# Performance work log

Measured on AMD Instinct MI355X. Metric: run time of the kernel, lower is better.

## Reference

```python
import jax, jax.numpy as jnp
import numpy as np

V = 32000      # vocab_size
CTX = 1024     # context_length
D = 768        # n_embd
H = 12         # n_heads
HD = D // H    # head_dim
L = 6          # n_layers
DFF = 4 * D
B, S = 2, 1024
EPS = 1e-5


def _layernorm(x, w, b):
    mu = jnp.mean(x, axis=-1, keepdims=True)
    var = jnp.mean(jnp.square(x - mu), axis=-1, keepdims=True)
    return (x - mu) * jax.lax.rsqrt(var + EPS) * w + b


def setup_inputs() -> dict:
    key = jax.random.key(0)
    ks = iter(jax.random.split(key, 32))
    s = 0.02
    idx = jax.random.randint(next(ks), (B, S), 0, V)
    p = {
        "idx": idx,
        "tok_emb": jax.random.normal(next(ks), (V, D), jnp.float32) * s,
        "pos_emb": jax.random.normal(next(ks), (CTX, D), jnp.float32) * s,
        "ln1_w": jnp.ones((L, D)), "ln1_b": jnp.zeros((L, D)),
        "Wq": jax.random.normal(next(ks), (L, D, D), jnp.float32) * s,
        "bq": jnp.zeros((L, D)),
        "Wk": jax.random.normal(next(ks), (L, D, D), jnp.float32) * s,
        "bk": jnp.zeros((L, D)),
        "Wv": jax.random.normal(next(ks), (L, D, D), jnp.float32) * s,
        "bv": jnp.zeros((L, D)),
        "Wo": jax.random.normal(next(ks), (L, D, D), jnp.float32) * s,
        "bo": jnp.zeros((L, D)),
        "ln2_w": jnp.ones((L, D)), "ln2_b": jnp.zeros((L, D)),
        "W1": jax.random.normal(next(ks), (L, D, DFF), jnp.float32) * s,
        "b1": jnp.zeros((L, DFF)),
        "W2": jax.random.normal(next(ks), (L, DFF, D), jnp.float32) * s,
        "b2": jnp.zeros((L, D)),
        "lnf_w": jnp.ones((D,)), "lnf_b": jnp.zeros((D,)),
        "lm_head_w": jax.random.normal(next(ks), (D, V), jnp.float32) * s,
    }
    return p


def _forward(idx, tok_emb, pos_emb, ln1_w, ln1_b, Wq, bq, Wk, bk, Wv, bv,
             Wo, bo, ln2_w, ln2_b, W1, b1, W2, b2, lnf_w, lnf_b, lm_head_w):
    b, s = idx.shape
    x = tok_emb[idx] + pos_emb[:s]  # [B,S,D]
    mask = jnp.tril(jnp.ones((s, s), dtype=bool))  # causal
    scale = 1.0 / np.sqrt(HD)
    for l in range(L):
        # --- attention ---
        h = _layernorm(x, ln1_w[l], ln1_b[l])
        q = (h @ Wq[l] + bq[l]).reshape(b, s, H, HD).transpose(0, 2, 1, 3)
        k = (h @ Wk[l] + bk[l]).reshape(b, s, H, HD).transpose(0, 2, 1, 3)
        v = (h @ Wv[l] + bv[l]).reshape(b, s, H, HD).transpose(0, 2, 1, 3)
        att = jnp.einsum('bhqd,bhkd->bhqk', q, k) * scale
        att = jnp.where(mask, att, -jnp.inf)
        att = jax.nn.softmax(att, axis=-1)
        y = jnp.einsum('bhqk,bhkd->bhqd', att, v)
        y = y.transpose(0, 2, 1, 3).reshape(b, s, D)
        x = x + y @ Wo[l] + bo[l]
        # --- MLP ---
        h2 = _layernorm(x, ln2_w[l], ln2_b[l])
        x = x + jax.nn.relu(h2 @ W1[l] + b1[l]) @ W2[l] + b2[l]
    logits = _layernorm(x, lnf_w, lnf_b) @ lm_head_w  # [B,S,V]
    return logits


def reference(idx, tok_emb, pos_emb, ln1_w, ln1_b, Wq, bq, Wk, bk, Wv, bv,
              Wo, bo, ln2_w, ln2_b, W1, b1, W2, b2, lnf_w, lnf_b, lm_head_w):
    return _forward(idx, tok_emb, pos_emb, ln1_w, ln1_b, Wq, bq, Wk, bk, Wv,
                    bv, Wo, bo, ln2_w, ln2_b, W1, b1, W2, b2, lnf_w, lnf_b,
                    lm_head_w)
```

## Files before the change

### kernel.cpp

```cpp
#include <hip/hip_runtime.h>
#include <hip/hip_bf16.h>
#include <math.h>

#define D 768
#define NH 12
#define HD 64
#define NL 6
#define DFF 3072
#define BB 2
#define SS 1024
#define NROWS (BB*SS)
#define VOCAB 32000
#define QKVN (3*D)
#define LN_EPS 1e-5f

typedef __attribute__((ext_vector_type(8))) short bf16x8;
typedef __attribute__((ext_vector_type(4))) float f32x4;

typedef __attribute__((address_space(1))) const unsigned char* gas_ptr;
typedef __attribute__((address_space(3))) unsigned char* las_ptr;

__device__ __forceinline__ void load_lds16(const void* g, void* l) {
    __builtin_amdgcn_global_load_lds((gas_ptr)g, (las_ptr)l, 16, 0, 0);
}

__device__ __forceinline__ void storeOut(float* p, float v) { *p = v; }
__device__ __forceinline__ void storeOut(__hip_bfloat16* p, float v) { *p = __float2bfloat16(v); }
__device__ __forceinline__ ushort f2bs(float f) {
    __hip_bfloat16 h = __float2bfloat16(f);
    return *(ushort*)&h;
}

#define WAIT_VMCNT(n) asm volatile("s_waitcnt vmcnt(" #n ")" ::: "memory")

__global__ void embed_kernel(const int* __restrict__ idx, const float* __restrict__ tok,
                             const float* __restrict__ pos, float* __restrict__ x) {
    int row = blockIdx.x;
    int s = row % SS;
    int t = idx[row];
    for (int c = threadIdx.x; c < D; c += blockDim.x)
        x[row*D + c] = tok[(size_t)t*D + c] + pos[s*D + c];
}

template<typename OT>
__global__ __launch_bounds__(256) void layernorm_kernel(const float* __restrict__ x,
                                                        const float* __restrict__ w,
                                                        const float* __restrict__ b,
                                                        OT* __restrict__ out) {
    int row = blockIdx.x;
    __shared__ float l1[4], l2[4];
    int base = row * D;
    float vals[3];
    float s1 = 0.f, s2 = 0.f;
#pragma unroll
    for (int i = 0; i < 3; i++) {
        float v = x[base + threadIdx.x + i*256];
        vals[i] = v; s1 += v; s2 += v*v;
    }
#pragma unroll
    for (int o = 32; o > 0; o >>= 1) {
        s1 += __shfl_down(s1, o, 64);
        s2 += __shfl_down(s2, o, 64);
    }
    if ((threadIdx.x & 63) == 0) { l1[threadIdx.x >> 6] = s1; l2[threadIdx.x >> 6] = s2; }
    __syncthreads();
    float sum   = l1[0] + l1[1] + l1[2] + l1[3];
    float sumsq = l2[0] + l2[1] + l2[2] + l2[3];
    float mu  = sum * (1.f / D);
    float var = sumsq * (1.f / D) - mu * mu;
    float inv = rsqrtf(var + LN_EPS);
#pragma unroll
    for (int i = 0; i < 3; i++) {
        int c = threadIdx.x + i*256;
        storeOut(&out[base + c], (vals[i] - mu) * inv * w[c] + b[c]);
    }
}

__global__ __launch_bounds__(256) void transpose_cvt(const float* __restrict__ src,
                                                     __hip_bfloat16* __restrict__ dst,
                                                     int K, int N,
                                                     size_t srcLayerStride, size_t dstLayerStride,
                                                     int dstRowOff) {
    int l = blockIdx.z;
    src += (size_t)l * srcLayerStride;
    dst += (size_t)l * dstLayerStride + (size_t)dstRowOff * K;
    __shared__ float t[32][33];
    int k0 = blockIdx.x*32, n0 = blockIdx.y*32;
    int tx = threadIdx.x & 31, ty = threadIdx.x >> 5;
    for (int i = ty; i < 32; i += 8) t[i][tx] = src[(size_t)(k0+i)*N + n0+tx];
    __syncthreads();
    for (int i = ty; i < 32; i += 8) dst[(size_t)(n0+i)*K + k0+tx] = __float2bfloat16(t[tx][i]);
}

__global__ __launch_bounds__(256) void qkvo_trans(const float* __restrict__ Wq,
                                                  const float* __restrict__ Wk,
                                                  const float* __restrict__ Wv,
                                                  const float* __restrict__ Wo,
                                                  __hip_bfloat16* __restrict__ qkvT,
                                                  __hip_bfloat16* __restrict__ WoT) {
    int z = blockIdx.z, l = z >> 2, m = z & 3;
    const float* src = (m==0 ? Wq : m==1 ? Wk : m==2 ? Wv : Wo) + (size_t)l*D*D;
    __hip_bfloat16* dst = (m < 3) ? qkvT + (size_t)l*QKVN*D + (size_t)m*D*D
                                  : WoT  + (size_t)l*D*D;
    __shared__ float t[32][33];
    int k0 = blockIdx.x*32, n0 = blockIdx.y*32;
    int tx = threadIdx.x & 31, ty = threadIdx.x >> 5;
    for (int i = ty; i < 32; i += 8) t[i][tx] = src[(size_t)(k0+i)*D + n0+tx];
    __syncthreads();
    for (int i = ty; i < 32; i += 8) dst[(size_t)(n0+i)*D + k0+tx] = __float2bfloat16(t[tx][i]);
}

__global__ void pack_qkv_bias(const float* __restrict__ bq, const float* __restrict__ bk,
                              const float* __restrict__ bv, float* __restrict__ dst) {
    int l = blockIdx.y;
    int i = blockIdx.x*256 + threadIdx.x;
    dst[l*QKVN + i]         = bq[l*D + i];
    dst[l*QKVN + D + i]     = bk[l*D + i];
    dst[l*QKVN + 2*D + i]   = bv[l*D + i];
}

#define GSTAGE(buf, k0) do {                                                     \
    _Pragma("unroll")                                                            \
    for (int i_ = 0; i_ < BM/64; i_++) {                                         \
        int rt_ = wid*(BM/4) + i_*16;                                            \
        load_lds16(A + (size_t)(bm + rt_ + lrow)*K + (k0) + lcol,                \
                   &As[buf][rt_][0]);                                            \
    }                                                                            \
    _Pragma("unroll")                                                            \
    for (int i_ = 0; i_ < BN/64; i_++) {                                         \
        int rt_ = wid*(BN/4) + i_*16;                                            \
        load_lds16(BT + (size_t)(bn + rt_ + lrow)*K + (k0) + lcol,               \
                   &Bs[buf][rt_][0]);                                            \
    } } while (0)

template<int BM, int BN, int CMAJ, typename OT, int RELU, int RESID, int HASB, int VSTORE>
__global__ __launch_bounds__(256) void gemm_mfma(const ushort* __restrict__ A,
                                                 const ushort* __restrict__ BT,
                                                 const float* __restrict__ bias,
                                                 const float* __restrict__ X,
                                                 OT* __restrict__ C,
                                                 ushort* __restrict__ vt,
                                                 int N, int K, int gx, int gy) {
    constexpr int WTM = BM/2, WTN = BN/2;
    constexpr int FRM = BM/32, FRN = BN/32;
    constexpr int LPS = BM/64 + BN/64;
    __shared__ ushort As[3][BM][32];
    __shared__ ushort Bs[3][BN][32];

    int id = blockIdx.x;
    int swz = (id & 7) * (gridDim.x >> 3) + (id >> 3);
    int bx, by;
    if (CMAJ) { bx = swz / gy; by = swz - bx * gy; }
    else      { by = swz / gx; bx = swz - by * gx; }
    int bm = by * BM, bn = bx * BN;

    int tid = threadIdx.x;
    int lane = tid & 63, wid = tid >> 6;
    int wr = wid >> 1, wc = wid & 1;
    int lrow = lane >> 2;
    int lcol = (((lane & 3) ^ (lrow & 3)) * 8);
    int fr = lane & 15, fc = lane >> 4;

    f32x4 acc[FRM][FRN];
#pragma unroll
    for (int i = 0; i < FRM; i++)
#pragma unroll
        for (int j = 0; j < FRN; j++)
#pragma unroll
            for (int r = 0; r < 4; r++) acc[i][j][r] = 0.f;

    const int NT = K / 32;
    GSTAGE(0, 0);
    GSTAGE(1, 32);

    int cur = 0;
    for (int t = 0; t < NT; t++) {
        if (t + 1 < NT) {
            if constexpr (LPS == 2) WAIT_VMCNT(2);
            else if constexpr (LPS == 3) WAIT_VMCNT(3);
            else WAIT_VMCNT(4);
        } else {
            WAIT_VMCNT(0);
        }
        __builtin_amdgcn_s_barrier();
        asm volatile("" ::: "memory");
        if (t + 2 < NT) {
            int nb = cur >= 1 ? cur - 1 : cur + 2;
            GSTAGE(nb, (t+2)*32);
        }
        bf16x8 af[FRM], bf[FRN];
#pragma unroll
        for (int mi = 0; mi < FRM; mi++)
            af[mi] = *(const bf16x8*)&As[cur][wr*WTM + mi*16 + fr][(fc ^ (fr & 3))*8];
#pragma unroll
        for (int ni = 0; ni < FRN; ni++)
            bf[ni] = *(const bf16x8*)&Bs[cur][wc*WTN + ni*16 + fr][(fc ^ (fr & 3))*8];
        __builtin_amdgcn_s_setprio(1);
#pragma unroll
        for (int mi = 0; mi < FRM; mi++)
#pragma unroll
            for (int ni = 0; ni < FRN; ni++)
                acc[mi][ni] = __builtin_amdgcn_mfma_f32_16x16x32_bf16(af[mi], bf[ni], acc[mi][ni], 0, 0, 0);
        __builtin_amdgcn_s_setprio(0);
        cur = cur < 2 ? cur + 1 : 0;
    }

    if (VSTORE && bn >= 2*D) {
        int hh = (bn - 2*D) / HD;
        int b  = bm >> 10;
        size_t vbase = ((size_t)(b*NH + hh)) * HD;
        int srow0 = (bm & (SS-1)) + wr*WTM + fc*4;
#pragma unroll
        for (int mi = 0; mi < FRM; mi++) {
#pragma unroll
            for (int ni = 0; ni < FRN; ni++) {
                int col = bn + wc*WTN + ni*16 + fr;
                int d   = wc*WTN + ni*16 + fr;
                float bv_ = bias[col];
                ushort4 u;
                u.x = f2bs(acc[mi][ni][0] + bv_);
                u.y = f2bs(acc[mi][ni][1] + bv_);
                u.z = f2bs(acc[mi][ni][2] + bv_);
                u.w = f2bs(acc[mi][ni][3] + bv_);
                *(ushort4*)&vt[(vbase + d)*SS + srow0 + mi*16] = u;
            }
        }
    } else {
#pragma unroll
        for (int mi = 0; mi < FRM; mi++) {
#pragma unroll
            for (int r = 0; r < 4; r++) {
                int row = bm + wr*WTM + mi*16 + fc*4 + r;
#pragma unroll
                for (int ni = 0; ni < FRN; ni++) {
                    int col = bn + wc*WTN + ni*16 + fr;
                    float v = acc[mi][ni][r];
                    if (HASB) v += bias[col];
                    if (RESID) v += X[(size_t)row * N + col];
                    if (RELU) v = fmaxf(v, 0.f);
                    storeOut(&C[(size_t)row * N + col], v);
                }
            }
        }
    }
}

#define KVSTAGE(buf, kv0) do {                                                   \
    _Pragma("unroll")                                                            \
    for (int j_ = 0; j_ < 2; j_++) {                                             \
        int r_ = w*16 + j_*8 + srow8;                                            \
        load_lds16(qkv + (size_t)(b*SS + (kv0) + r_)*QKVN + D + h*HD + schunk*8, \
                   &Ks[buf][w*16 + j_*8][0]);                                    \
        load_lds16(vt + ((size_t)(b*NH + h)*HD + r_)*SS + (kv0) + schunk*8,      \
                   &Vs[buf][w*16 + j_*8][0]);                                    \
    } } while (0)

__global__ __launch_bounds__(256) void attn_mfma(const ushort* __restrict__ qkv,
                                                 const ushort* __restrict__ vt,
                                                 __hip_bfloat16* __restrict__ y) {
    const int bx = blockIdx.x;
    const int qt = 15 - (bx & 15);
    const int h  = (bx >> 4) % NH;
    const int b  = bx / (16*NH);
    const int tid  = threadIdx.x;
    const int lane = tid & 63, w = tid >> 6;
    const int fr = lane & 15, fc = lane >> 4;

    __shared__ ushort Qs[64][64];
    __shared__ ushort Ks[2][64][64];
    __shared__ ushort Vs[2][64][64];
    __shared__ ushort Ps[4][16][72];

    const int q0 = qt * 64;
    const int srow8  = lane >> 3;
    const int schunk = (lane & 7) ^ srow8;

#pragma unroll
    for (int j = 0; j < 2; j++) {
        int r = w*16 + j*8 + srow8;
        load_lds16(qkv + (size_t)(b*SS + q0 + r)*QKVN + h*HD + schunk*8, &Qs[w*16 + j*8][0]);
    }
    KVSTAGE(0, 0);
    asm volatile("s_waitcnt vmcnt(0)" ::: "memory");
    __syncthreads();
    bf16x8 qf[2];
#pragma unroll
    for (int s = 0; s < 2; s++)
        qf[s] = *(const bf16x8*)&Qs[w*16 + fr][((s*4 + fc) ^ (fr & 7))*8];

    f32x4 oacc[4];
#pragma unroll
    for (int ni = 0; ni < 4; ni++)
#pragma unroll
        for (int r = 0; r < 4; r++) oacc[ni][r] = 0.f;
    float m[4] = {-INFINITY, -INFINITY, -INFINITY, -INFINITY};
    float l[4] = {0.f, 0.f, 0.f, 0.f};

    int cur = 0;
    for (int kt = 0; kt <= qt; kt++) {
        if (kt < qt) KVSTAGE(cur^1, (kt+1)*64);
        f32x4 sacc[4];
#pragma unroll
        for (int ni = 0; ni < 4; ni++)
#pragma unroll
            for (int r = 0; r < 4; r++) sacc[ni][r] = 0.f;
#pragma unroll
        for (int ni = 0; ni < 4; ni++)
#pragma unroll
            for (int s = 0; s < 2; s++) {
                bf16x8 kf = *(const bf16x8*)&Ks[cur][ni*16 + fr][((s*4 + fc) ^ (fr & 7))*8];
                sacc[ni] = __builtin_amdgcn_mfma_f32_16x16x32_bf16(qf[s], kf, sacc[ni], 0, 0, 0);
            }
        if (kt == qt) {
#pragma unroll
            for (int ni = 0; ni < 4; ni++)
#pragma unroll
                for (int r = 0; r < 4; r++) {
                    float v = sacc[ni][r] * 0.125f;
                    sacc[ni][r] = (ni*16 + fr > w*16 + fc*4 + r) ? -INFINITY : v;
                }
        } else {
#pragma unroll
            for (int ni = 0; ni < 4; ni++)
#pragma unroll
                for (int r = 0; r < 4; r++) sacc[ni][r] *= 0.125f;
        }
        float p[4][4];
#pragma unroll
        for (int r = 0; r < 4; r++) {
            float mx = fmaxf(fmaxf(sacc[0][r], sacc[1][r]), fmaxf(sacc[2][r], sacc[3][r]));
#pragma unroll
            for (int o = 1; o < 16; o <<= 1) mx = fmaxf(mx, __shfl_xor(mx, o, 64));
            float mn = fmaxf(m[r], mx);
            float fac = __expf(m[r] - mn);
            float rs = 0.f;
#pragma unroll
            for (int ni = 0; ni < 4; ni++) {
                float pv = __expf(sacc[ni][r] - mn);
                p[ni][r] = pv;
                rs += pv;
            }
#pragma unroll
            for (int o = 1; o < 16; o <<= 1) rs += __shfl_xor(rs, o, 64);
            l[r] = l[r] * fac + rs;
            m[r] = mn;
#pragma unroll
            for (int ni = 0; ni < 4; ni++) oacc[ni][r] *= fac;
        }
#pragma unroll
        for (int ni = 0; ni < 4; ni++)
#pragma unroll
            for (int r = 0; r < 4; r++)
                Ps[w][fc*4 + r][ni*16 + fr] = f2bs(p[ni][r]);
        bf16x8 pa[2];
#pragma unroll
        for (int s = 0; s < 2; s++) pa[s] = *(const bf16x8*)&Ps[w][fr][s*32 + fc*8];
#pragma unroll
        for (int ni = 0; ni < 4; ni++)
#pragma unroll
            for (int s = 0; s < 2; s++) {
                bf16x8 vf = *(const bf16x8*)&Vs[cur][ni*16 + fr][((s*4 + fc) ^ (fr & 7))*8];
                oacc[ni] = __builtin_amdgcn_mfma_f32_16x16x32_bf16(pa[s], vf, oacc[ni], 0, 0, 0);
            }
        asm volatile("s_waitcnt vmcnt(0)" ::: "memory");
        __syncthreads();
        cur ^= 1;
    }
#pragma unroll
    for (int r = 0; r < 4; r++) {
        float rinv = 1.f / l[r];
        int row = b*SS + q0 + w*16 + fc*4 + r;
#pragma unroll
        for (int ni = 0; ni < 4; ni++)
            y[(size_t)row*D + h*HD + ni*16 + fr] = __float2bfloat16(oacc[ni][r] * rinv);
    }
}

extern "C" void kernel_launch(void* const* d_in, const int* in_sizes, int n_in,
                              void* d_out, int out_size, void* d_ws, size_t ws_size,
                              hipStream_t stream) {
    const int*   idx  = (const int*)d_in[0];
    const float* tok  = (const float*)d_in[1];
    const float* pos  = (const float*)d_in[2];
    const float* ln1w = (const float*)d_in[3];
    const float* ln1b = (const float*)d_in[4];
    const float* Wq   = (const float*)d_in[5];
    const float* bq   = (const float*)d_in[6];
    const float* Wk   = (const float*)d_in[7];
    const float* bk   = (const float*)d_in[8];
    const float* Wv   = (const float*)d_in[9];
    const float* bv   = (const float*)d_in[10];
    const float* Wo   = (const float*)d_in[11];
    const float* bo   = (const float*)d_in[12];
    const float* ln2w = (const float*)d_in[13];
    const float* ln2b = (const float*)d_in[14];
    const float* W1   = (const float*)d_in[15];
    const float* b1   = (const float*)d_in[16];
    const float* W2   = (const float*)d_in[17];
    const float* b2   = (const float*)d_in[18];
    const float* lnfw = (const float*)d_in[19];
    const float* lnfb = (const float*)d_in[20];
    const float* lmw  = (const float*)d_in[21];
    float* out = (float*)d_out;

    char* p = (char*)d_ws;
    __hip_bfloat16* qkvT = (__hip_bfloat16*)p; p += (size_t)NL*QKVN*D*2;
    __hip_bfloat16* WoT  = (__hip_bfloat16*)p; p += (size_t)NL*D*D*2;
    __hip_bfloat16* W1T  = (__hip_bfloat16*)p; p += (size_t)NL*DFF*D*2;
    __hip_bfloat16* W2T  = (__hip_bfloat16*)p; p += (size_t)NL*D*DFF*2;
    __hip_bfloat16* lmT  = (__hip_bfloat16*)p; p += (size_t)VOCAB*D*2;
    float*          bqkv = (float*)p;          p += (size_t)NL*QKVN*4;
    float*          x    = (float*)p;          p += (size_t)NROWS*D*4;
    __hip_bfloat16* h    = (__hip_bfloat16*)p; p += (size_t)NROWS*D*2;
    __hip_bfloat16* qkv  = (__hip_bfloat16*)p; p += (size_t)NROWS*QKVN*2;
    __hip_bfloat16* vt   = (__hip_bfloat16*)p; p += (size_t)BB*NH*HD*SS*2;
    __hip_bfloat16* yb   = (__hip_bfloat16*)p; p += (size_t)NROWS*D*2;
    __hip_bfloat16* a1   = (__hip_bfloat16*)p; p += (size_t)NROWS*DFF*2;

    qkvo_trans<<<dim3(D/32, D/32, NL*4), 256, 0, stream>>>(Wq, Wk, Wv, Wo, qkvT, WoT);
    transpose_cvt<<<dim3(D/32, DFF/32, NL), 256, 0, stream>>>(W1, W1T, D, DFF, (size_t)D*DFF, (size_t)DFF*D, 0);
    transpose_cvt<<<dim3(DFF/32, D/32, NL), 256, 0, stream>>>(W2, W2T, DFF, D, (size_t)DFF*D, (size_t)D*DFF, 0);
    transpose_cvt<<<dim3(D/32, VOCAB/32, 1), 256, 0, stream>>>(lmw, lmT, D, VOCAB, 0, 0, 0);
    pack_qkv_bias<<<dim3(3, NL), 256, 0, stream>>>(bq, bk, bv, bqkv);

    embed_kernel<<<NROWS, 256, 0, stream>>>(idx, tok, pos, x);

    for (int l = 0; l < NL; l++) {
        layernorm_kernel<<<NROWS, 256, 0, stream>>>(x, ln1w + l*D, ln1b + l*D, h);
        gemm_mfma<128,64,0,__hip_bfloat16,0,0,1,1><<<576, 256, 0, stream>>>(
            (const ushort*)h, (const ushort*)(qkvT + (size_t)l*QKVN*D),
            bqkv + (size_t)l*QKVN, nullptr, qkv, (ushort*)vt, QKVN, D, QKVN/64, NROWS/128);
        attn_mfma<<<BB*NH*(SS/64), 256, 0, stream>>>((const ushort*)qkv, (const ushort*)vt, yb);
        gemm_mfma<64,64,0,float,0,1,1,0><<<384, 256, 0, stream>>>(
            (const ushort*)yb, (const ushort*)(WoT + (size_t)l*D*D),
            bo + (size_t)l*D, x, x, nullptr, D, D, D/64, NROWS/64);
        layernorm_kernel<<<NROWS, 256, 0, stream>>>(x, ln2w + l*D, ln2b + l*D, h);
        gemm_mfma<128,128,0,__hip_bfloat16,1,0,1,0><<<384, 256, 0, stream>>>(
            (const ushort*)h, (const ushort*)(W1T + (size_t)l*DFF*D),
            b1 + (size_t)l*DFF, nullptr, a1, nullptr, DFF, D, DFF/128, NROWS/128);
        gemm_mfma<64,64,0,float,0,1,1,0><<<384, 256, 0, stream>>>(
            (const ushort*)a1, (const ushort*)(W2T + (size_t)l*D*DFF),
            b2 + (size_t)l*D, x, x, nullptr, D, DFF, D/64, NROWS/64);
    }
    layernorm_kernel<<<NROWS, 256, 0, stream>>>(x, lnfw, lnfb, h);
    gemm_mfma<128,128,1,float,0,0,0,0><<<4000, 256, 0, stream>>>(
        (const ushort*)h, (const ushort*)lmT, nullptr, nullptr, out, nullptr, VOCAB, D,
        VOCAB/128, NROWS/128);
}
```

Baseline: 1.251 ms.

## Add 256x256 LM-head GEMM kernel and simplify generic GEMM to double buffering

Adds a dedicated LM-head GEMM that uses 256x256 tiles with 512 threads, a K-step of 64, XOR-swizzled LDS and two-stage prefetch, so each block reuses more data and fewer blocks are launched for the largest matmul. It also changes the generic gemm_mfma from a three-buffer pipeline with partial vmcnt waits to a plain double buffer that waits for all loads and syncs on every iteration. That second change may add stalls to every per-layer GEMM, while the large LM-head tile costs more registers and LDS per block and lowers occupancy.

```diff
diff --git a/kernel.cpp b/kernel.cpp
--- a/kernel.cpp
+++ b/kernel.cpp
@@ -143,9 +143,8 @@
                                                  int N, int K, int gx, int gy) {
     constexpr int WTM = BM/2, WTN = BN/2;
     constexpr int FRM = BM/32, FRN = BN/32;
-    constexpr int LPS = BM/64 + BN/64;
-    __shared__ ushort As[3][BM][32];
-    __shared__ ushort Bs[3][BN][32];
+    __shared__ ushort As[2][BM][32];
+    __shared__ ushort Bs[2][BN][32];
 
     int id = blockIdx.x;
     int swz = (id & 7) * (gridDim.x >> 3) + (id >> 3);
@@ -169,25 +168,13 @@
 #pragma unroll
             for (int r = 0; r < 4; r++) acc[i][j][r] = 0.f;
 
-    const int NT = K / 32;
     GSTAGE(0, 0);
-    GSTAGE(1, 32);
+    asm volatile("s_waitcnt vmcnt(0)" ::: "memory");
+    __syncthreads();
 
     int cur = 0;
-    for (int t = 0; t < NT; t++) {
-        if (t + 1 < NT) {
-            if constexpr (LPS == 2) WAIT_VMCNT(2);
-            else if constexpr (LPS == 3) WAIT_VMCNT(3);
-            else WAIT_VMCNT(4);
-        } else {
-            WAIT_VMCNT(0);
-        }
-        __builtin_amdgcn_s_barrier();
-        asm volatile("" ::: "memory");
-        if (t + 2 < NT) {
-            int nb = cur >= 1 ? cur - 1 : cur + 2;
-            GSTAGE(nb, (t+2)*32);
-        }
+    for (int t = 0; t < K/32; t++) {
+        if (t*32 + 32 < K) GSTAGE(cur^1, t*32 + 32);
         bf16x8 af[FRM], bf[FRN];
 #pragma unroll
         for (int mi = 0; mi < FRM; mi++)
@@ -202,7 +189,9 @@
             for (int ni = 0; ni < FRN; ni++)
                 acc[mi][ni] = __builtin_amdgcn_mfma_f32_16x16x32_bf16(af[mi], bf[ni], acc[mi][ni], 0, 0, 0);
         __builtin_amdgcn_s_setprio(0);
-        cur = cur < 2 ? cur + 1 : 0;
+        asm volatile("s_waitcnt vmcnt(0)" ::: "memory");
+        __syncthreads();
+        cur ^= 1;
     }
 
     if (VSTORE && bn >= 2*D) {
@@ -243,6 +232,92 @@
             }
         }
     }
+}
+
+#define LGS(buf, k0) do {                                                         \
+    _Pragma("unroll")                                                             \
+    for (int i_ = 0; i_ < 4; i_++) {                                              \
+        int li_ = i_*512 + tid;                                                   \
+        int row_ = li_ >> 3;                                                      \
+        int kc_ = ((li_ & 7) ^ (row_ & 7)) * 8;                                   \
+        size_t doff_ = (size_t)(i_*512 + wid*64) * 8;                             \
+        load_lds16(A  + (size_t)(bm + row_)*D + (k0) + kc_,                       \
+                   (ushort*)As + (size_t)(buf)*256*64 + doff_);                   \
+        load_lds16(BT + (size_t)(bn + row_)*D + (k0) + kc_,                       \
+                   (ushort*)Bs + (size_t)(buf)*256*64 + doff_);                   \
+    } } while (0)
+
+__global__ __launch_bounds__(512) void lm256_gemm(const ushort* __restrict__ A,
+                                                  const ushort* __restrict__ BT,
+                                                  float* __restrict__ C) {
+    constexpr int NT = D / 64;
+    __shared__ ushort As[2][256][64];
+    __shared__ ushort Bs[2][256][64];
+
+    int id = blockIdx.x;
+    int swz = (id & 7) * 125 + (id >> 3);
+    int by = swz & 7;
+    int bx = swz >> 3;
+    int bm = by * 256, bn = bx * 256;
+
+    int tid = threadIdx.x;
+    int lane = tid & 63, wid = tid >> 6;
+    int wr = wid >> 2, wc = wid & 3;
+    int fr = lane & 15, fc = lane >> 4;
+
+    f32x4 acc[8][4];
+#pragma unroll
+    for (int i = 0; i < 8; i++)
+#pragma unroll
+        for (int j = 0; j < 4; j++)
+#pragma unroll
+            for (int r = 0; r < 4; r++) acc[i][j][r] = 0.f;
+
+    LGS(0, 0);
+    LGS(1, 64);
+    WAIT_VMCNT(8);
+    __builtin_amdgcn_s_barrier();
+
+    for (int t = 0; t < NT; t++) {
+        int buf = t & 1;
+        bf16x8 bfr[2][4];
+#pragma unroll
+        for (int kk = 0; kk < 2; kk++)
+#pragma unroll
+            for (int ni = 0; ni < 4; ni++)
+                bfr[kk][ni] = *(const bf16x8*)&Bs[buf][wc*64 + ni*16 + fr][((kk*4 + fc) ^ (fr & 7))*8];
+        __builtin_amdgcn_s_setprio(1);
+#pragma unroll
+        for (int mi = 0; mi < 8; mi++) {
+            bf16x8 a0 = *(const bf16x8*)&As[buf][wr*128 + mi*16 + fr][((0 + fc) ^ (fr & 7))*8];
+            bf16x8 a1 = *(const bf16x8*)&As[buf][wr*128 + mi*16 + fr][((4 + fc) ^ (fr & 7))*8];
+#pragma unroll
+            for (int ni = 0; ni < 4; ni++) {
+                acc[mi][ni] = __builtin_amdgcn_mfma_f32_16x16x32_bf16(a0, bfr[0][ni], acc[mi][ni], 0, 0, 0);
+                acc[mi][ni] = __builtin_amdgcn_mfma_f32_16x16x32_bf16(a1, bfr[1][ni], acc[mi][ni], 0, 0, 0);
+            }
+        }
+        __builtin_amdgcn_s_setprio(0);
+        __builtin_amdgcn_s_barrier();
+        asm volatile("" ::: "memory");
+        if (t + 2 < NT) LGS(buf, (t+2)*64);
+        if (t + 1 < NT) {
+            if (t + 2 < NT) WAIT_VMCNT(8);
+            else            WAIT_VMCNT(0);
+            __builtin_amdgcn_s_barrier();
+        }
+    }
+
+#pragma unroll
+    for (int mi = 0; mi < 8; mi++)
+#pragma unroll
+        for (int r = 0; r < 4; r++) {
+            int row = bm + wr*128 + mi*16 + fc*4 + r;
+            float* cp = C + (size_t)row * VOCAB + bn + wc*64 + fr;
+#pragma unroll
+            for (int ni = 0; ni < 4; ni++)
+                cp[ni*16] = acc[mi][ni][r];
+        }
 }
 
 #define KVSTAGE(buf, kv0) do {                                                   \
@@ -443,7 +518,5 @@
             b2 + (size_t)l*D, x, x, nullptr, D, DFF, D/64, NROWS/64);
     }
     layernorm_kernel<<<NROWS, 256, 0, stream>>>(x, lnfw, lnfb, h);
-    gemm_mfma<128,128,1,float,0,0,0,0><<<4000, 256, 0, stream>>>(
-        (const ushort*)h, (const ushort*)lmT, nullptr, nullptr, out, nullptr, VOCAB, D,
-        VOCAB/128, NROWS/128);
-}
+    lm256_gemm<<<1000, 512, 0, stream>>>((const ushort*)h, (const ushort*)lmT, out);
+}
```

Result: no change. 1.243 ms (-0.7%).
